# Performance work log

Hardware: AMD Instinct MI355X
Metric: run time of the kernel (lower is better)

## Reference

```python
import jax, jax.numpy as jnp
import numpy as np

B, S, L, E, H, T, V, D = 32, 256, 24, 300, 256, 16, 50000, 256  # batch, sents, words/sent, emb, gru_units, topics, vocab, dense


def setup_inputs() -> dict:
    key = jax.random.key(0)
    ks = jax.random.split(key, 12)
    word_ids = jax.random.randint(ks[0], (B, S, L), 0, V, dtype=jnp.int32)
    tsize = S // T
    starts = (jnp.arange(T, dtype=jnp.int32) * tsize + 1)          # 1-indexed inclusive
    ends = (jnp.arange(T, dtype=jnp.int32) * tsize + tsize)
    topic_start_ends = jnp.broadcast_to(jnp.stack([starts, ends], -1)[None], (B, T, 2))
    g = lambda k, shape, sc=0.05: (jax.random.normal(k, shape, jnp.float32) * sc)
    return {
        "word_ids": word_ids,
        "topic_start_ends": topic_start_ends,
        "emb": g(ks[1], (V, E), 0.1),
        "Wih_f": g(ks[2], (3 * H, E)), "Whh_f": g(ks[3], (3 * H, H)),
        "bih_f": jnp.zeros((3 * H,), jnp.float32), "bhh_f": jnp.zeros((3 * H,), jnp.float32),
        "Wih_b": g(ks[4], (3 * H, E)), "Whh_b": g(ks[5], (3 * H, H)),
        "bih_b": jnp.zeros((3 * H,), jnp.float32), "bhh_b": jnp.zeros((3 * H,), jnp.float32),
        "W_att": g(ks[6], (4 * H, 4 * H)), "v_att": g(ks[7], (4 * H, 1)),
        "W_dna": g(ks[8], (4 * H, D)), "b_dna": jnp.zeros((D,), jnp.float32),
        "W_out": g(ks[9], (D, 1)), "b_out": jnp.zeros((1,), jnp.float32),
    }


def _gru_dir(x, Wih, Whh, bih, bhh, reverse):
    # x: [B, S, E] -> outputs [B, S, H], final hidden [B, H]  (PyTorch GRU cell math)
    def step(h, xt):
        gi = xt @ Wih.T + bih
        gh = h @ Whh.T + bhh
        ir, iz, inn = jnp.split(gi, 3, axis=-1)
        hr, hz, hn = jnp.split(gh, 3, axis=-1)
        r = jax.nn.sigmoid(ir + hr)
        z = jax.nn.sigmoid(iz + hz)
        n = jnp.tanh(inn + r * hn)
        h2 = (1.0 - z) * n + z * h
        return h2, h2
    h0 = jnp.zeros((x.shape[0], Whh.shape[1]), x.dtype)
    hT, ys = jax.lax.scan(step, h0, jnp.swapaxes(x, 0, 1), reverse=reverse)
    return jnp.swapaxes(ys, 0, 1), hT


def _gather_seq(x, idx):
    # x: [B, S', C], idx: [B, K] -> [B, K, C]
    return jnp.take_along_axis(x, idx[:, :, None].astype(jnp.int32), axis=1)


def reference(word_ids, topic_start_ends, emb, Wih_f, Whh_f, bih_f, bhh_f,
              Wih_b, Whh_b, bih_b, bhh_b, W_att, v_att, W_dna, b_dna, W_out, b_out):
    # --- sent_encoder: per-sentence mean of word embeddings ---
    sent_vecs = jnp.mean(emb[word_ids], axis=2)  # [B, S, E]

    # --- doc_encoder: bidirectional GRU ---
    out_f, hT_f = _gru_dir(sent_vecs, Wih_f, Whh_f, bih_f, bhh_f, reverse=False)
    out_b, hT_b = _gru_dir(sent_vecs, Wih_b, Whh_b, bih_b, bhh_b, reverse=True)
    sent_rep = jnp.concatenate([out_f, out_b], axis=-1)          # [B, S, 2H]
    hidden = jnp.stack([hT_f, hT_b], axis=0)                     # [2, B, H]
    # faithful to torch: hidden.view(batch_size, 2H) (row-major reshape)
    doc_vec = hidden.reshape(B, 2 * H)
    doc_rep = jnp.broadcast_to(doc_vec[:, None, :], (B, S, 2 * H))

    # --- topic representation via boundary differencing on front/back-padded output ---
    padded = jnp.pad(sent_rep, ((0, 0), (1, 1), (0, 0)))         # [B, S+2, 2H]
    starts = topic_start_ends[..., 0]                            # [B, T], 1-indexed
    ends = topic_start_ends[..., 1]
    topic_fwd = _gather_seq(padded, ends)[..., :H] - _gather_seq(padded, starts - 1)[..., :H]
    topic_bwd = _gather_seq(padded, starts)[..., H:] - _gather_seq(padded, ends + 1)[..., H:]
    topic_mat = jnp.concatenate([topic_fwd, topic_bwd], axis=-1)  # [B, T, 2H]
    # sentence s (0-indexed) -> topic t with starts[t] <= s+1 <= ends[t]
    sent_1idx = jnp.arange(1, S + 1, dtype=jnp.int32)
    topic_id = jax.vmap(lambda e: jnp.searchsorted(e, sent_1idx, side='left'))(ends)  # [B, S]
    topic_rep = jnp.take_along_axis(topic_mat, topic_id[:, :, None], axis=1)          # [B, S, 2H]

    # --- decoder_attention ---
    cat_ds = jnp.concatenate([doc_rep, sent_rep], axis=-1)       # [B, S, 4H]
    cat_ts = jnp.concatenate([topic_rep, sent_rep], axis=-1)
    doc_scores = jnp.tanh(cat_ds @ W_att) @ v_att                # [B, S, 1]
    topic_scores = jnp.tanh(cat_ts @ W_att) @ v_att
    doc_w = jax.nn.softmax(doc_scores, axis=1)
    topic_w = jax.nn.softmax(topic_scores, axis=1)
    context = doc_w * doc_rep + topic_w * topic_rep              # [B, S, 2H]
    inp = jnp.concatenate([sent_rep, context], axis=-1)          # [B, S, 4H]
    h = jax.nn.relu(inp @ W_dna + b_dna)                         # dropout is identity (eval)
    logits = (h @ W_out + b_out)[..., 0]                         # [B, S]
    return logits
```

## Files before the change

kernel.cpp:

```cpp
#include <hip/hip_runtime.h>
#include <hip/hip_bf16.h>
#include <math.h>

#define Bd 32
#define Sd 256
#define Ld 24
#define Ed 300
#define Hd 256
#define Td 16
#define Dd 256
#define EP 320

using short8 = __attribute__((ext_vector_type(8))) short;
using f32x4  = __attribute__((ext_vector_type(4))) float;

__device__ __forceinline__ float fsigm(float x) { return 1.f / (1.f + __expf(-x)); }
__device__ __forceinline__ float ftanh(float x) {
  float e = __expf(2.f * x);
  return 1.f - 2.f / (e + 1.f);
}

__global__ void sent_means_kernel(const int* __restrict__ wids,
                                  const float* __restrict__ emb,
                                  __hip_bfloat16* __restrict__ apad) {
  int r = blockIdx.x;
  __shared__ int ids[Ld];
  int tid = threadIdx.x;
  if (tid < Ld) ids[tid] = wids[r * Ld + tid];
  __syncthreads();
  float acc = 0.f;
  if (tid < Ed) {
#pragma unroll
    for (int w = 0; w < Ld; ++w) acc += emb[(size_t)ids[w] * Ed + tid];
    acc *= (1.f / 24.f);
  }
  apad[r * EP + tid] = __float2bfloat16(tid < Ed ? acc : 0.f);
}

__global__ void prep1_kernel(const float* __restrict__ wih_f, const float* __restrict__ wih_b,
                             const float* __restrict__ whh_f, const float* __restrict__ whh_b,
                             __hip_bfloat16* __restrict__ wpadf, __hip_bfloat16* __restrict__ wpadb,
                             __hip_bfloat16* __restrict__ whhbf_f, __hip_bfloat16* __restrict__ whhbf_b) {
  int i = blockIdx.x * 512 + threadIdx.x;
  const int PW = 768 * EP;
  const int WH = 768 * Hd;
  if (i < 2 * PW) {
    const float* src = (i < PW) ? wih_f : wih_b;
    __hip_bfloat16* dst = (i < PW) ? wpadf : wpadb;
    int j = (i < PW) ? i : i - PW;
    int n = j / EP, k = j % EP;
    dst[j] = __float2bfloat16(k < Ed ? src[n * Ed + k] : 0.f);
  } else {
    int j = i - 2 * PW;
    const float* src = (j < WH) ? whh_f : whh_b;
    __hip_bfloat16* dst = (j < WH) ? whhbf_f : whhbf_b;
    int k = (j < WH) ? j : j - WH;
    dst[k] = __float2bfloat16(src[k]);
  }
}

__global__ __launch_bounds__(256) void gemm_xwt_kernel(
    const __hip_bfloat16* __restrict__ A, int lda,
    const __hip_bfloat16* __restrict__ W, int ldw,
    float* __restrict__ C, int ldc,
    int M, int N, int K,
    const float* __restrict__ bias) {
  __shared__ unsigned short la[64][32];
  __shared__ unsigned short lb[64][32];
  const int tid = threadIdx.x;
  const int m0 = blockIdx.x * 64, n0 = blockIdx.y * 64;
  const int lane = tid & 63, wid = tid >> 6;
  const int wm = (wid >> 1) * 32, wn = (wid & 1) * 32;
  const int lrow = tid >> 2, lcol = (tid & 3) * 8;
  f32x4 acc00 = {0.f, 0.f, 0.f, 0.f}, acc01 = {0.f, 0.f, 0.f, 0.f};
  f32x4 acc10 = {0.f, 0.f, 0.f, 0.f}, acc11 = {0.f, 0.f, 0.f, 0.f};
  int arow = m0 + lrow; if (arow > M - 1) arow = M - 1;
  const int brow = n0 + lrow;
  const int fr = lane & 15, fq = (lane >> 4) * 8;
  for (int k0 = 0; k0 < K; k0 += 32) {
    uint4 av = *(const uint4*)(A + (size_t)arow * lda + k0 + lcol);
    uint4 bv = *(const uint4*)(W + (size_t)brow * ldw + k0 + lcol);
    *(uint4*)(&la[lrow][lcol]) = av;
    *(uint4*)(&lb[lrow][lcol]) = bv;
    __syncthreads();
    short8 a0 = *(const short8*)(&la[wm + fr][fq]);
    short8 a1 = *(const short8*)(&la[wm + 16 + fr][fq]);
    short8 b0 = *(const short8*)(&lb[wn + fr][fq]);
    short8 b1 = *(const short8*)(&lb[wn + 16 + fr][fq]);
    acc00 = __builtin_amdgcn_mfma_f32_16x16x32_bf16(a0, b0, acc00, 0, 0, 0);
    acc01 = __builtin_amdgcn_mfma_f32_16x16x32_bf16(a0, b1, acc01, 0, 0, 0);
    acc10 = __builtin_amdgcn_mfma_f32_16x16x32_bf16(a1, b0, acc10, 0, 0, 0);
    acc11 = __builtin_amdgcn_mfma_f32_16x16x32_bf16(a1, b1, acc11, 0, 0, 0);
    __syncthreads();
  }
  const int rq = (lane >> 4) * 4;
  f32x4 accs[2][2] = {{acc00, acc01}, {acc10, acc11}};
  for (int i = 0; i < 2; ++i)
    for (int j = 0; j < 2; ++j) {
      int n = n0 + wn + j * 16 + fr;
      float bv = bias ? bias[n] : 0.f;
      for (int r2 = 0; r2 < 4; ++r2) {
        int m = m0 + wm + i * 16 + rq + r2;
        if (m < M) C[(size_t)m * ldc + n] = accs[i][j][r2] + bv;
      }
    }
}

__global__ __launch_bounds__(512, 1) void gru_mfma_kernel(
    const float* __restrict__ gi_f, const float* __restrict__ gi_b,
    const __hip_bfloat16* __restrict__ whhbf_f, const __hip_bfloat16* __restrict__ whhbf_b,
    const float* __restrict__ bhh_f, const float* __restrict__ bhh_b,
    float* __restrict__ sent_rep, __hip_bfloat16* __restrict__ sent_rep_bf,
    float* __restrict__ hT_f, float* __restrict__ hT_b,
    const float* __restrict__ w_att, const float* __restrict__ w_dna,
    __hip_bfloat16* __restrict__ wpack1, __hip_bfloat16* __restrict__ wpack2) {
  __shared__ float gi_lds[2][8][768];
  __shared__ __hip_bfloat16 h_bf[2][256];
  __shared__ float gh[768];
  __shared__ float stg32[2][8][256];
  const int blk = blockIdx.x;
  const int tid = threadIdx.x;

  if (blk >= 64) {
    const size_t q = (size_t)(blk - 64) * 512 + tid;
    size_t flat = q * 8;
    const size_t HALF = (size_t)1280 * 512;
    const bool second = flat >= HALF;
    size_t r = second ? flat - HALF : flat;
    int n = (int)(r >> 9), k0 = (int)(r & 511);
    __hip_bfloat16* dst = second ? wpack2 : wpack1;
#pragma unroll
    for (int j = 0; j < 8; ++j) {
      int k = k0 + j;
      float v;
      if (!second)
        v = (n < 1024) ? w_att[(size_t)k * 1024 + n]
                       : w_dna[(size_t)(512 + k) * 256 + (n - 1024)];
      else
        v = (n < 1024) ? w_att[(size_t)(512 + k) * 1024 + n]
                       : w_dna[(size_t)k * 256 + (n - 1024)];
      dst[(size_t)n * 512 + k] = __float2bfloat16(v);
    }
    return;
  }

  const int dir = blk >> 5, b = blk & 31;
  const int lane = tid & 63, w = tid >> 6;
  const float* gi = dir ? gi_b : gi_f;
  const __hip_bfloat16* whh = dir ? whhbf_b : whhbf_f;
  const float* bhh = dir ? bhh_b : bhh_f;

  {
#pragma unroll
    for (int i = 0; i < 3; ++i) {
      int idx = tid + i * 512;
      int u = idx / 192;
      int c4 = (idx - u * 192) * 4;
      int s = dir ? (255 - u) : u;
      const float* g = gi + (size_t)(((b << 8) + s) * 768 + c4);
      __builtin_amdgcn_global_load_lds(
          (const __attribute__((address_space(1))) unsigned int*)g,
          (__attribute__((address_space(3))) unsigned int*)&gi_lds[0][u][c4], 16, 0, 0);
    }
  }
  if (tid < 256) h_bf[0][tid] = __float2bfloat16(0.f);

  const int fr = lane & 15, kq = (lane >> 4) * 8;
  short8 bfrag[6][8];
  {
    const int n0 = w * 96 + fr;
#pragma unroll
    for (int nt = 0; nt < 6; ++nt)
#pragma unroll
      for (int kt = 0; kt < 8; ++kt)
        bfrag[nt][kt] = *(const short8*)(whh + (size_t)(n0 + nt * 16) * 256 + kt * 32 + kq);
  }

  float bhr = 0.f, bhz = 0.f, bhn = 0.f, hprev = 0.f;
  if (tid < 256) { bhr = bhh[tid]; bhz = bhh[256 + tid]; bhn = bhh[512 + tid]; }

  asm volatile("s_waitcnt vmcnt(0) lgkmcnt(0)\n\ts_barrier" ::: "memory");

  for (int t = 0; t < Sd; ++t) {
    const int rb = t & 1, wb = rb ^ 1;

    float gl0 = 0.f, gl1 = 0.f, gl2 = 0.f;
    if (tid < 256) {
      const float* gl = gi_lds[(t >> 3) & 1][t & 7];
      gl0 = gl[tid]; gl1 = gl[256 + tid]; gl2 = gl[512 + tid];
    }

    f32x4 acc[6];
#pragma unroll
    for (int nt = 0; nt < 6; ++nt) acc[nt] = (f32x4){0.f, 0.f, 0.f, 0.f};
#pragma unroll
    for (int kt = 0; kt < 8; ++kt) {
      short8 av = *(const short8*)(&h_bf[rb][kt * 32 + kq]);
#pragma unroll
      for (int nt = 0; nt < 6; ++nt)
        acc[nt] = __builtin_amdgcn_mfma_f32_16x16x32_bf16(av, bfrag[nt][kt], acc[nt], 0, 0, 0);
      __builtin_amdgcn_sched_group_barrier(0x100, 1, 0);
      __builtin_amdgcn_sched_group_barrier(0x008, 6, 0);
    }
    if (lane < 16) {
#pragma unroll
      for (int nt = 0; nt < 6; ++nt) gh[w * 96 + nt * 16 + lane] = acc[nt][0];
    }
    asm volatile("s_waitcnt lgkmcnt(0)\n\ts_barrier" ::: "memory");

    if (tid < 256) {
      float rr = fsigm(gl0 + gh[tid] + bhr);
      float zz = fsigm(gl1 + gh[256 + tid] + bhz);
      float nn = ftanh(gl2 + rr * (gh[512 + tid] + bhn));
      float hn = (1.f - zz) * nn + zz * hprev;
      hprev = hn;
      h_bf[wb][tid] = __float2bfloat16(hn);
      stg32[(t >> 3) & 1][t & 7][tid] = hn;
    } else if ((t & 7) == 0) {
      if (t + 8 < Sd) {
        const int buf = ((t >> 3) + 1) & 1;
#pragma unroll
        for (int i = 0; i < 6; ++i) {
          int idx = (tid - 256) + i * 256;
          int u = idx / 192;
          int c4 = (idx - u * 192) * 4;
          int s = dir ? (255 - (t + 8 + u)) : (t + 8 + u);
          const float* g = gi + (size_t)(((b << 8) + s) * 768 + c4);
          __builtin_amdgcn_global_load_lds(
              (const __attribute__((address_space(1))) unsigned int*)g,
              (__attribute__((address_space(3))) unsigned int*)&gi_lds[buf][u][c4], 16, 0, 0);
        }
      }
      if (t >= 8) {
        const int base = t - 8;
        const int gp = ((t >> 3) - 1) & 1;
        const int d = tid - 256;
#pragma unroll
        for (int u = 0; u < 8; ++u) {
          int sg = dir ? (255 - (base + u)) : (base + u);
          size_t rowg = (size_t)((b << 8) + sg);
          int col = dir ? (256 + d) : d;
          float v = stg32[gp][u][d];
          sent_rep[rowg * 512 + col] = v;
          sent_rep_bf[rowg * 512 + col] = __float2bfloat16(v);
        }
      }
    }
    if (w >= 4 && (t & 7) == 7)
      asm volatile("s_waitcnt vmcnt(0)" ::: "memory");
    asm volatile("s_waitcnt lgkmcnt(0)\n\ts_barrier" ::: "memory");
  }

  if (w >= 4) {
    const int base = 248, d = tid - 256;
#pragma unroll
    for (int u = 0; u < 8; ++u) {
      int sg = dir ? (255 - (base + u)) : (base + u);
      size_t rowg = (size_t)((b << 8) + sg);
      int col = dir ? (256 + d) : d;
      float v = stg32[1][u][d];
      sent_rep[rowg * 512 + col] = v;
      sent_rep_bf[rowg * 512 + col] = __float2bfloat16(v);
    }
  } else {
    (dir ? hT_b : hT_f)[b * 256 + tid] = hprev;
  }
}

__global__ void docvec_kernel(const float* __restrict__ hTf, const float* __restrict__ hTb,
                              __hip_bfloat16* __restrict__ dv) {
  int b = blockIdx.x, jj = threadIdx.x;
  int idx = b * 512 + jj;
  int dsel = idx >> 13;
  int rem = idx & 8191;
  int bp = rem >> 8, hp = rem & 255;
  float v = (dsel ? hTb : hTf)[bp * Hd + hp];
  dv[idx] = __float2bfloat16(v);
}

__global__ void topic_kernel(const int* __restrict__ tse, const float* __restrict__ sent_rep,
                             __hip_bfloat16* __restrict__ topic_bf) {
  int bt = blockIdx.x;
  int b = bt >> 4;
  int st = tse[bt * 2], en = tse[bt * 2 + 1];
  int dd = threadIdx.x;
  auto pad = [&](int i, int col) -> float {
    if (i < 1 || i > Sd) return 0.f;
    return sent_rep[((size_t)((b << 8) + (i - 1))) * 512 + col];
  };
  float fwd = pad(en, dd) - pad(st - 1, dd);
  float bwd = pad(st, Hd + dd) - pad(en + 1, Hd + dd);
  topic_bf[(size_t)bt * 512 + dd] = __float2bfloat16(fwd);
  topic_bf[(size_t)bt * 512 + Hd + dd] = __float2bfloat16(bwd);
}

__global__ void scores_kernel(const float* __restrict__ PD, const float* __restrict__ RT,
                              const float* __restrict__ QU, const float* __restrict__ v_att,
                              const int* __restrict__ tse,
                              float* __restrict__ dsc, float* __restrict__ tsc) {
  int r = blockIdx.x;
  int b = r >> 8, s = r & 255;
  int tid = threadIdx.x;
  int tsel = Td - 1;
  for (int t = 0; t < Td; ++t) {
    if (tse[(b * Td + t) * 2 + 1] >= s + 1) { tsel = t; break; }
  }
  const float* q = QU + (size_t)r * 1280;
  const float* p = PD + (size_t)b * 1280;
  const float* rr = RT + (size_t)(b * Td + tsel) * 1280;
  float accd = 0.f, acct = 0.f;
  for (int n = tid; n < 1024; n += 256) {
    float qv = q[n];
    float vv = v_att[n];
    accd += ftanh(p[n] + qv) * vv;
    acct += ftanh(rr[n] + qv) * vv;
  }
  __shared__ float s1[256], s2[256];
  s1[tid] = accd; s2[tid] = acct;
  __syncthreads();
  for (int off = 128; off > 0; off >>= 1) {
    if (tid < off) { s1[tid] += s1[tid + off]; s2[tid] += s2[tid + off]; }
    __syncthreads();
  }
  if (tid == 0) { dsc[r] = s1[0]; tsc[r] = s2[0]; }
}

__global__ void softmax_kernel(const float* __restrict__ dsc, const float* __restrict__ tsc,
                               float* __restrict__ dw, float* __restrict__ tw) {
  int b = blockIdx.x, s = threadIdx.x;
  __shared__ float red[256];
  for (int which = 0; which < 2; ++which) {
    const float* src = which ? tsc : dsc;
    float v = src[b * Sd + s];
    red[s] = v; __syncthreads();
    for (int off = 128; off > 0; off >>= 1) {
      if (s < off) red[s] = fmaxf(red[s], red[s + off]);
      __syncthreads();
    }
    float m = red[0]; __syncthreads();
    float e = __expf(v - m);
    red[s] = e; __syncthreads();
    for (int off = 128; off > 0; off >>= 1) {
      if (s < off) red[s] += red[s + off];
      __syncthreads();
    }
    float sum = red[0]; __syncthreads();
    (which ? tw : dw)[b * Sd + s] = e / sum;
  }
}

__global__ void final_kernel(const float* __restrict__ QU, const float* __restrict__ PD,
                             const float* __restrict__ RT, const float* __restrict__ dw,
                             const float* __restrict__ tw, const float* __restrict__ b_dna,
                             const float* __restrict__ w_out,
                             const float* __restrict__ b_out,
                             const int* __restrict__ tse, float* __restrict__ out) {
  int r = blockIdx.x;
  int b = r >> 8, s = r & 255;
  int dd = threadIdx.x;
  int tsel = Td - 1;
  for (int t = 0; t < Td; ++t) {
    if (tse[(b * Td + t) * 2 + 1] >= s + 1) { tsel = t; break; }
  }
  float wdv = dw[b * Sd + s], wtv = tw[b * Sd + s];
  float x = QU[(size_t)r * 1280 + 1024 + dd] + wdv * PD[(size_t)b * 1280 + 1024 + dd] +
            wtv * RT[(size_t)(b * Td + tsel) * 1280 + 1024 + dd] + b_dna[dd];
  x = fmaxf(x, 0.f);
  float term = x * w_out[dd];
  __shared__ float red[256];
  red[dd] = term; __syncthreads();
  for (int off = 128; off > 0; off >>= 1) {
    if (dd < off) red[dd] += red[dd + off];
    __syncthreads();
  }
  if (dd == 0) out[r] = red[0] + b_out[0];
}

static void launch_gemm(const __hip_bfloat16* A, int lda, const __hip_bfloat16* W, int ldw,
                        float* C, int ldc, int M, int N, int K,
                        const float* bias, hipStream_t stream) {
  dim3 grid((M + 63) / 64, N / 64);
  gemm_xwt_kernel<<<grid, 256, 0, stream>>>(A, lda, W, ldw, C, ldc, M, N, K, bias);
}

extern "C" void kernel_launch(void* const* d_in, const int* in_sizes, int n_in,
                              void* d_out, int out_size, void* d_ws, size_t ws_size,
                              hipStream_t stream) {
  const int* word_ids = (const int*)d_in[0];
  const int* tse      = (const int*)d_in[1];
  const float* emb   = (const float*)d_in[2];
  const float* wih_f = (const float*)d_in[3];
  const float* whh_f = (const float*)d_in[4];
  const float* bih_f = (const float*)d_in[5];
  const float* bhh_f = (const float*)d_in[6];
  const float* wih_b = (const float*)d_in[7];
  const float* whh_b = (const float*)d_in[8];
  const float* bih_b = (const float*)d_in[9];
  const float* bhh_b = (const float*)d_in[10];
  const float* w_att = (const float*)d_in[11];
  const float* v_att = (const float*)d_in[12];
  const float* w_dna = (const float*)d_in[13];
  const float* b_dna = (const float*)d_in[14];
  const float* w_out = (const float*)d_in[15];
  const float* b_out = (const float*)d_in[16];
  float* out = (float*)d_out;
  char* ws = (char*)d_ws;

  const int M = Bd * Sd;

  size_t off = 0;
  auto alloc = [&](size_t sz) { size_t o = off; off += (sz + 255) & ~(size_t)255; return o; };
  size_t o_svbf   = alloc((size_t)M * EP * 2);
  size_t o_wpadf  = alloc((size_t)768 * EP * 2);
  size_t o_wpadb  = alloc((size_t)768 * EP * 2);
  size_t o_whhbf  = alloc((size_t)768 * Hd * 2 * 2);
  size_t o_wpack1 = alloc((size_t)1280 * 512 * 2);
  size_t o_wpack2 = alloc((size_t)1280 * 512 * 2);
  size_t o_hTf    = alloc((size_t)Bd * Hd * 4);
  size_t o_hTb    = alloc((size_t)Bd * Hd * 4);
  size_t o_dvbf   = alloc((size_t)Bd * 512 * 2);
  size_t o_topbf  = alloc((size_t)Bd * Td * 512 * 2);
  size_t o_PD     = alloc((size_t)Bd * 1280 * 4);
  size_t o_RT     = alloc((size_t)Bd * Td * 1280 * 4);
  size_t o_dsc    = alloc((size_t)Bd * Sd * 4);
  size_t o_tsc    = alloc((size_t)Bd * Sd * 4);
  size_t o_dw     = alloc((size_t)Bd * Sd * 4);
  size_t o_tw     = alloc((size_t)Bd * Sd * 4);
  size_t o_srep32 = alloc((size_t)M * 512 * 4);
  size_t o_srepbf = alloc((size_t)M * 512 * 2);
  size_t o_gif    = alloc((size_t)M * 768 * 4);
  size_t o_gib    = alloc((size_t)M * 768 * 4);
  size_t o_QU = o_gif;
  (void)ws_size;

  __hip_bfloat16* svbf   = (__hip_bfloat16*)(ws + o_svbf);
  __hip_bfloat16* wpadf  = (__hip_bfloat16*)(ws + o_wpadf);
  __hip_bfloat16* wpadb  = (__hip_bfloat16*)(ws + o_wpadb);
  __hip_bfloat16* whhbf_f = (__hip_bfloat16*)(ws + o_whhbf);
  __hip_bfloat16* whhbf_b = whhbf_f + 768 * Hd;
  __hip_bfloat16* wpack1 = (__hip_bfloat16*)(ws + o_wpack1);
  __hip_bfloat16* wpack2 = (__hip_bfloat16*)(ws + o_wpack2);
  float* hTf = (float*)(ws + o_hTf);
  float* hTb = (float*)(ws + o_hTb);
  __hip_bfloat16* dvbf  = (__hip_bfloat16*)(ws + o_dvbf);
  __hip_bfloat16* topbf = (__hip_bfloat16*)(ws + o_topbf);
  float* PD  = (float*)(ws + o_PD);
  float* RT  = (float*)(ws + o_RT);
  float* dsc = (float*)(ws + o_dsc);
  float* tsc = (float*)(ws + o_tsc);
  float* dw  = (float*)(ws + o_dw);
  float* tw  = (float*)(ws + o_tw);
  float* srep32 = (float*)(ws + o_srep32);
  __hip_bfloat16* srepbf = (__hip_bfloat16*)(ws + o_srepbf);
  float* gif = (float*)(ws + o_gif);
  float* gib = (float*)(ws + o_gib);
  float* QU  = (float*)(ws + o_QU);

  sent_means_kernel<<<M, EP, 0, stream>>>(word_ids, emb, svbf);
  prep1_kernel<<<1728, 512, 0, stream>>>(wih_f, wih_b, whh_f, whh_b,
                                         wpadf, wpadb, whhbf_f, whhbf_b);
  launch_gemm(svbf, EP, wpadf, EP, gif, 768, M, 768, EP, bih_f, stream);
  launch_gemm(svbf, EP, wpadb, EP, gib, 768, M, 768, EP, bih_b, stream);
  gru_mfma_kernel<<<384, 512, 0, stream>>>(gif, gib, whhbf_f, whhbf_b, bhh_f, bhh_b,
                                           srep32, srepbf, hTf, hTb,
                                           w_att, w_dna, wpack1, wpack2);
  docvec_kernel<<<Bd, 512, 0, stream>>>(hTf, hTb, dvbf);
  topic_kernel<<<Bd * Td, 256, 0, stream>>>(tse, srep32, topbf);
  launch_gemm(srepbf, 512, wpack2, 512, QU, 1280, M, 1280, 512, nullptr, stream);
  launch_gemm(dvbf, 512, wpack1, 512, PD, 1280, Bd, 1280, 512, nullptr, stream);
  launch_gemm(topbf, 512, wpack1, 512, RT, 1280, Bd * Td, 1280, 512, nullptr, stream);
  scores_kernel<<<M, 256, 0, stream>>>(PD, RT, QU, v_att, tse, dsc, tsc);
  softmax_kernel<<<Bd, 256, 0, stream>>>(dsc, tsc, dw, tw);
  final_kernel<<<M, 256, 0, stream>>>(QU, PD, RT, dw, tw, b_dna, w_out, b_out, tse, out);
}
```

Before: 575.3 us.

## Shrink GRU recurrence blocks to four waves and store hidden states directly

Each GRU block now runs 256 threads instead of 512. Each wave owns 12 n-tiles of the recurrent weight in registers, so every thread also does the gate math and issues the prefetch. The LDS staging buffer for hidden-state output and the double-buffered h are removed, and sent_rep is written to global memory every step. The aim is to cut barrier participants and idle helper waves in the latency-bound recurrence, at the cost of much higher VGPR pressure (96 short8 fragments per lane) and per-step global stores sitting on the critical path.

```diff
diff --git a/kernel.cpp b/kernel.cpp
--- a/kernel.cpp
+++ b/kernel.cpp
@@ -106,7 +106,7 @@
     }
 }
 
-__global__ __launch_bounds__(512, 1) void gru_mfma_kernel(
+__global__ __launch_bounds__(256, 1) void gru_mfma_kernel(
     const float* __restrict__ gi_f, const float* __restrict__ gi_b,
     const __hip_bfloat16* __restrict__ whhbf_f, const __hip_bfloat16* __restrict__ whhbf_b,
     const float* __restrict__ bhh_f, const float* __restrict__ bhh_b,
@@ -115,14 +115,13 @@
     const float* __restrict__ w_att, const float* __restrict__ w_dna,
     __hip_bfloat16* __restrict__ wpack1, __hip_bfloat16* __restrict__ wpack2) {
   __shared__ float gi_lds[2][8][768];
-  __shared__ __hip_bfloat16 h_bf[2][256];
+  __shared__ __hip_bfloat16 h_bf[256];
   __shared__ float gh[768];
-  __shared__ float stg32[2][8][256];
   const int blk = blockIdx.x;
   const int tid = threadIdx.x;
 
   if (blk >= 64) {
-    const size_t q = (size_t)(blk - 64) * 512 + tid;
+    const size_t q = (size_t)(blk - 64) * 256 + tid;
     size_t flat = q * 8;
     const size_t HALF = (size_t)1280 * 512;
     const bool second = flat >= HALF;
@@ -152,8 +151,8 @@
 
   {
 #pragma unroll
-    for (int i = 0; i < 3; ++i) {
-      int idx = tid + i * 512;
+    for (int i = 0; i < 6; ++i) {
+      int idx = tid + i * 256;
       int u = idx / 192;
       int c4 = (idx - u * 192) * 4;
       int s = dir ? (255 - u) : u;
@@ -163,108 +162,79 @@
           (__attribute__((address_space(3))) unsigned int*)&gi_lds[0][u][c4], 16, 0, 0);
     }
   }
-  if (tid < 256) h_bf[0][tid] = __float2bfloat16(0.f);
+  h_bf[tid] = __float2bfloat16(0.f);
 
   const int fr = lane & 15, kq = (lane >> 4) * 8;
-  short8 bfrag[6][8];
+  short8 bfrag[12][8];
   {
-    const int n0 = w * 96 + fr;
-#pragma unroll
-    for (int nt = 0; nt < 6; ++nt)
+    const int n0 = w * 192 + fr;
+#pragma unroll
+    for (int nt = 0; nt < 12; ++nt)
 #pragma unroll
       for (int kt = 0; kt < 8; ++kt)
         bfrag[nt][kt] = *(const short8*)(whh + (size_t)(n0 + nt * 16) * 256 + kt * 32 + kq);
   }
 
-  float bhr = 0.f, bhz = 0.f, bhn = 0.f, hprev = 0.f;
-  if (tid < 256) { bhr = bhh[tid]; bhz = bhh[256 + tid]; bhn = bhh[512 + tid]; }
+  const float bhr = bhh[tid], bhz = bhh[256 + tid], bhn = bhh[512 + tid];
+  float hprev = 0.f;
+
+  const int col = dir ? (256 + tid) : tid;
 
   asm volatile("s_waitcnt vmcnt(0) lgkmcnt(0)\n\ts_barrier" ::: "memory");
 
   for (int t = 0; t < Sd; ++t) {
-    const int rb = t & 1, wb = rb ^ 1;
-
-    float gl0 = 0.f, gl1 = 0.f, gl2 = 0.f;
-    if (tid < 256) {
-      const float* gl = gi_lds[(t >> 3) & 1][t & 7];
-      gl0 = gl[tid]; gl1 = gl[256 + tid]; gl2 = gl[512 + tid];
-    }
-
-    f32x4 acc[6];
-#pragma unroll
-    for (int nt = 0; nt < 6; ++nt) acc[nt] = (f32x4){0.f, 0.f, 0.f, 0.f};
+    const float* glp = gi_lds[(t >> 3) & 1][t & 7];
+    float gl0 = glp[tid], gl1 = glp[256 + tid], gl2 = glp[512 + tid];
+
+    f32x4 acc[12];
+#pragma unroll
+    for (int nt = 0; nt < 12; ++nt) acc[nt] = (f32x4){0.f, 0.f, 0.f, 0.f};
 #pragma unroll
     for (int kt = 0; kt < 8; ++kt) {
-      short8 av = *(const short8*)(&h_bf[rb][kt * 32 + kq]);
-#pragma unroll
-      for (int nt = 0; nt < 6; ++nt)
+      short8 av = *(const short8*)(&h_bf[kt * 32 + kq]);
+#pragma unroll
+      for (int nt = 0; nt < 12; ++nt)
         acc[nt] = __builtin_amdgcn_mfma_f32_16x16x32_bf16(av, bfrag[nt][kt], acc[nt], 0, 0, 0);
-      __builtin_amdgcn_sched_group_barrier(0x100, 1, 0);
-      __builtin_amdgcn_sched_group_barrier(0x008, 6, 0);
     }
     if (lane < 16) {
 #pragma unroll
-      for (int nt = 0; nt < 6; ++nt) gh[w * 96 + nt * 16 + lane] = acc[nt][0];
+      for (int nt = 0; nt < 12; ++nt) gh[w * 192 + nt * 16 + lane] = acc[nt][0];
     }
     asm volatile("s_waitcnt lgkmcnt(0)\n\ts_barrier" ::: "memory");
 
-    if (tid < 256) {
-      float rr = fsigm(gl0 + gh[tid] + bhr);
-      float zz = fsigm(gl1 + gh[256 + tid] + bhz);
-      float nn = ftanh(gl2 + rr * (gh[512 + tid] + bhn));
-      float hn = (1.f - zz) * nn + zz * hprev;
-      hprev = hn;
-      h_bf[wb][tid] = __float2bfloat16(hn);
-      stg32[(t >> 3) & 1][t & 7][tid] = hn;
-    } else if ((t & 7) == 0) {
-      if (t + 8 < Sd) {
-        const int buf = ((t >> 3) + 1) & 1;
-#pragma unroll
-        for (int i = 0; i < 6; ++i) {
-          int idx = (tid - 256) + i * 256;
-          int u = idx / 192;
-          int c4 = (idx - u * 192) * 4;
-          int s = dir ? (255 - (t + 8 + u)) : (t + 8 + u);
-          const float* g = gi + (size_t)(((b << 8) + s) * 768 + c4);
-          __builtin_amdgcn_global_load_lds(
-              (const __attribute__((address_space(1))) unsigned int*)g,
-              (__attribute__((address_space(3))) unsigned int*)&gi_lds[buf][u][c4], 16, 0, 0);
-        }
+    if ((t & 7) == 7) {
+      asm volatile("s_waitcnt vmcnt(0)" ::: "memory");
+    }
+    float rr = fsigm(gl0 + gh[tid] + bhr);
+    float zz = fsigm(gl1 + gh[256 + tid] + bhz);
+    float nn = ftanh(gl2 + rr * (gh[512 + tid] + bhn));
+    float hn = (1.f - zz) * nn + zz * hprev;
+    hprev = hn;
+    h_bf[tid] = __float2bfloat16(hn);
+    {
+      const int s = dir ? (255 - t) : t;
+      const size_t rowg = (size_t)((b << 8) + s);
+      sent_rep[rowg * 512 + col] = hn;
+      sent_rep_bf[rowg * 512 + col] = __float2bfloat16(hn);
+    }
+    if ((t & 7) == 0 && t + 8 < Sd) {
+      const int buf = ((t >> 3) + 1) & 1;
+#pragma unroll
+      for (int i = 0; i < 6; ++i) {
+        int idx = tid + i * 256;
+        int u = idx / 192;
+        int c4 = (idx - u * 192) * 4;
+        int s = dir ? (255 - (t + 8 + u)) : (t + 8 + u);
+        const float* g = gi + (size_t)(((b << 8) + s) * 768 + c4);
+        __builtin_amdgcn_global_load_lds(
+            (const __attribute__((address_space(1))) unsigned int*)g,
+            (__attribute__((address_space(3))) unsigned int*)&gi_lds[buf][u][c4], 16, 0, 0);
       }
-      if (t >= 8) {
-        const int base = t - 8;
-        const int gp = ((t >> 3) - 1) & 1;
-        const int d = tid - 256;
-#pragma unroll
-        for (int u = 0; u < 8; ++u) {
-          int sg = dir ? (255 - (base + u)) : (base + u);
-          size_t rowg = (size_t)((b << 8) + sg);
-          int col = dir ? (256 + d) : d;
-          float v = stg32[gp][u][d];
-          sent_rep[rowg * 512 + col] = v;
-          sent_rep_bf[rowg * 512 + col] = __float2bfloat16(v);
-        }
-      }
-    }
-    if (w >= 4 && (t & 7) == 7)
-      asm volatile("s_waitcnt vmcnt(0)" ::: "memory");
+    }
     asm volatile("s_waitcnt lgkmcnt(0)\n\ts_barrier" ::: "memory");
   }
 
-  if (w >= 4) {
-    const int base = 248, d = tid - 256;
-#pragma unroll
-    for (int u = 0; u < 8; ++u) {
-      int sg = dir ? (255 - (base + u)) : (base + u);
-      size_t rowg = (size_t)((b << 8) + sg);
-      int col = dir ? (256 + d) : d;
-      float v = stg32[1][u][d];
-      sent_rep[rowg * 512 + col] = v;
-      sent_rep_bf[rowg * 512 + col] = __float2bfloat16(v);
-    }
-  } else {
-    (dir ? hT_b : hT_f)[b * 256 + tid] = hprev;
-  }
+  (dir ? hT_b : hT_f)[b * 256 + tid] = hprev;
 }
 
 __global__ void docvec_kernel(const float* __restrict__ hTf, const float* __restrict__ hTb,
@@ -461,7 +431,7 @@
                                          wpadf, wpadb, whhbf_f, whhbf_b);
   launch_gemm(svbf, EP, wpadf, EP, gif, 768, M, 768, EP, bih_f, stream);
   launch_gemm(svbf, EP, wpadb, EP, gib, 768, M, 768, EP, bih_b, stream);
-  gru_mfma_kernel<<<384, 512, 0, stream>>>(gif, gib, whhbf_f, whhbf_b, bhh_f, bhh_b,
+  gru_mfma_kernel<<<704, 256, 0, stream>>>(gif, gib, whhbf_f, whhbf_b, bhh_f, bhh_b,
                                            srep32, srepbf, hTf, hTb,
                                            w_att, w_dna, wpack1, wpack2);
   docvec_kernel<<<Bd, 512, 0, stream>>>(hTf, hTb, dvbf);
```

Measured after the change: 688.0 us. 19.6% more time.
